# Kernel optimization log

Hardware: AMD Instinct MI355X
Metric: run time of the kernel (lower is better)

The kernel has to match this reference:

```python
import jax, jax.numpy as jnp
import numpy as np

# Material / problem parameters (from init_kwargs)
G_C = 0.0027
L_0 = 0.015
PF_TOL = 0.01
ENERGY_SCALING = 1.0
NU = 0.3
E_MOD = 210.0
LAM = E_MOD * NU / ((1.0 + NU) * (1.0 - 2.0 * NU))
MU = E_MOD / (2.0 * (1.0 + NU))
K_MOD = LAM + 2.0 * MU / 3.0  # bulk modulus for vol/dev split

N_NODES = 263169
N_ELEMS = 262144
N_IP = 4
NN = 4  # nodes per element


def setup_inputs() -> dict:
    key = jax.random.key(0)
    ks = jax.random.split(key, 9)
    u = jax.random.normal(ks[0], (N_NODES,), dtype=jnp.float32) * 0.01
    v = jax.random.normal(ks[1], (N_NODES,), dtype=jnp.float32) * 0.01
    c = jax.random.uniform(ks[2], (N_NODES,), dtype=jnp.float32)
    prev_c = jax.random.uniform(ks[3], (N_NODES,), dtype=jnp.float32)
    connectivities = jax.random.randint(ks[4], (N_ELEMS, NN), 0, N_NODES, dtype=jnp.int32)
    N = jax.random.uniform(ks[5], (N_ELEMS, N_IP, NN), dtype=jnp.float32)
    N = N / jnp.sum(N, axis=-1, keepdims=True)  # shape functions sum to 1
    dNdx = jax.random.normal(ks[6], (N_ELEMS, N_IP, 2, NN), dtype=jnp.float32)
    B = jax.random.normal(ks[7], (N_ELEMS, N_IP, 3, 2 * NN), dtype=jnp.float32)
    volumes = jax.random.uniform(ks[8], (N_ELEMS, N_IP), dtype=jnp.float32)
    return {"u": u, "v": v, "c": c, "prev_c": prev_c,
            "connectivities": connectivities, "N": N, "dNdx": dNdx,
            "B": B, "volumes": volumes}


def reference(u, v, c, prev_c, connectivities, N, dNdx, B, volumes):
    # --- phase-field gather + degradation -------------------------------
    c_el = c[connectivities]                     # [E, nn] irregular gather
    one_minus_c_el = 1.0 - c_el                  # c_elemental in source
    one_minus_c_ip = jnp.einsum('ein,en->ei', N, one_minus_c_el)  # [E, ip]
    ip_g = one_minus_c_ip ** 2                   # degradation g = (1-c)^2

    # --- fracture (AT2) energy density ----------------------------------
    c_ip = 1.0 - one_minus_c_ip
    grad_c = jnp.einsum('eidn,en->eid', dNdx, c_el)  # [E, ip, 2]
    frac_density = (G_C / (2.0 * L_0)) * (c_ip ** 2 + (L_0 ** 2) * jnp.sum(grad_c ** 2, axis=-1))
    E_fracture = jnp.sum(frac_density * volumes)

    # --- irreversibility penalty ----------------------------------------
    penalty = G_C / L_0 * (1.0 / PF_TOL ** 2 - 1.0) * ENERGY_SCALING
    E_irr = jnp.sum(0.5 * penalty * jax.nn.relu(prev_c - c) ** 2)

    # --- B-matrix strain transform --------------------------------------
    u_el = u[connectivities]                     # [E, nn]
    v_el = v[connectivities]                     # [E, nn]
    uv = jnp.stack((u_el, v_el), axis=-1).reshape(u_el.shape[0], 2 * NN)  # interleaved dofs
    strain = jnp.einsum('eikn,en->eik', B, uv)   # Voigt [E, ip, 3]
    exx, eyy, gxy = strain[..., 0], strain[..., 1], strain[..., 2]
    exy = 0.5 * gxy
    tr = exx + eyy                               # plane strain: ezz = 0

    # --- vol/dev (Amor) split energy parts ------------------------------
    dev_xx = exx - tr / 3.0
    dev_yy = eyy - tr / 3.0
    dev_zz = -tr / 3.0
    dev2 = dev_xx ** 2 + dev_yy ** 2 + dev_zz ** 2 + 2.0 * exy ** 2
    tr_pos = jnp.maximum(tr, 0.0)
    tr_neg = jnp.minimum(tr, 0.0)
    psi_plus = 0.5 * K_MOD * tr_pos ** 2 + MU * dev2
    psi_minus = 0.5 * K_MOD * tr_neg ** 2

    ip_strain_energy = (psi_plus * ip_g + psi_minus) * volumes
    E_elastic = jnp.sum(ip_strain_energy)
    return (E_elastic, E_fracture, E_irr)
```

## Files before the change

kernel.cpp:

```cpp
#include <hip/hip_runtime.h>

namespace {
constexpr int N_ELEMS  = 262144;
constexpr int N_NODES  = 263169;
constexpr int BLK      = 256;
constexpr int EPB      = 64;
constexpr int NBLOCKS  = N_ELEMS / EPB;
constexpr int PACK_BLOCKS = (N_NODES + BLK - 1) / BLK;

constexpr long long WS2_F4   = 263232;
constexpr long long P_EL_OFF = WS2_F4 * 4;
constexpr long long P_IR_OFF = P_EL_OFF + 2LL * NBLOCKS;

constexpr float GC_2L0  = 0.09f;
constexpr float L0SQ    = 0.015f * 0.015f;
constexpr float MU_     = 80.76923076923077f;
constexpr float K_MOD   = 175.0f;
constexpr float PENALTY = 1799.82f;
}

typedef float vfloat4 __attribute__((ext_vector_type(4)));

__device__ __forceinline__ float waveReduce(float x) {
#pragma unroll
    for (int off = 32; off; off >>= 1) x += __shfl_down(x, off, 64);
    return x;
}

__global__ __launch_bounds__(256) void pack_nodes(
    const float* __restrict__ u, const float* __restrict__ v,
    const float* __restrict__ c, const float* __restrict__ prev_c,
    float* __restrict__ ws2, float* __restrict__ partialsI)
{
    const int i = blockIdx.x * BLK + threadIdx.x;
    float Eirr = 0.f;
    if (i < N_NODES) {
        const float ci = c[i], ui = u[i], vi = v[i];
        const float d = fmaxf(prev_c[i] - ci, 0.f);
        Eirr = 0.5f * PENALTY * d * d;
        vfloat4 r; r.x = ci; r.y = ui; r.z = vi; r.w = 0.f;
        __builtin_nontemporal_store(r, reinterpret_cast<vfloat4*>(ws2) + i);
    }
    Eirr = waveReduce(Eirr);
    __shared__ float sI[4];
    const int lane = threadIdx.x & 63, wid = threadIdx.x >> 6;
    if (lane == 0) sI[wid] = Eirr;
    __syncthreads();
    if (threadIdx.x == 0)
        partialsI[blockIdx.x] = sI[0] + sI[1] + sI[2] + sI[3];
}

__global__ __launch_bounds__(256) void fused_energy(
    const int* __restrict__ conn,
    const float* __restrict__ Nf, const float* __restrict__ dNdx,
    const float* __restrict__ B, const float* __restrict__ vol,
    const float* __restrict__ ws2, float* __restrict__ partials)
{
    __shared__ vfloat4 ldsB[24 * 65];
    __shared__ vfloat4 ldsD[2 * 257];

    const int k     = threadIdx.x;
    const int ebase = blockIdx.x * EPB;
    const vfloat4* Bf4 = reinterpret_cast<const vfloat4*>(B);
    const vfloat4* Df4 = reinterpret_cast<const vfloat4*>(dNdx);
    const vfloat4* Nf4 = reinterpret_cast<const vfloat4*>(Nf);
    const vfloat4* W4  = reinterpret_cast<const vfloat4*>(ws2);

    const vfloat4* Bg = Bf4 + (long long)ebase * 24;
#pragma unroll
    for (int r = 0; r < 6; ++r) {
        const int j = k + BLK * r;
        ldsB[(j % 24) * 65 + (j / 24)] = Bg[j];
    }
    const vfloat4* Dg = Df4 + (long long)ebase * 8;
#pragma unroll
    for (int r = 0; r < 2; ++r) {
        const int j = k + BLK * r;
        ldsD[(j & 1) * 257 + (j >> 1)] = Dg[j];
    }

    const int idx = conn[4ll * ebase + k];
    const vfloat4 nv = W4[idx];

    const vfloat4 Nr  = Nf4[4ll * ebase + k];
    const float   vip = vol[4ll * ebase + k];

    const int base = k & ~3;
    const float c0 = __shfl(nv.x, base),     c1 = __shfl(nv.x, base + 1);
    const float c2 = __shfl(nv.x, base + 2), c3 = __shfl(nv.x, base + 3);
    const float u0 = __shfl(nv.y, base),     u1 = __shfl(nv.y, base + 1);
    const float u2 = __shfl(nv.y, base + 2), u3 = __shfl(nv.y, base + 3);
    const float v0 = __shfl(nv.z, base),     v1 = __shfl(nv.z, base + 1);
    const float v2 = __shfl(nv.z, base + 2), v3 = __shfl(nv.z, base + 3);

    __syncthreads();

    const int m = k >> 2, ip = k & 3;
    const vfloat4 dx = ldsD[k], dy = ldsD[257 + k];
    const vfloat4 b0 = ldsB[(6 * ip + 0) * 65 + m];
    const vfloat4 b1 = ldsB[(6 * ip + 1) * 65 + m];
    const vfloat4 b2 = ldsB[(6 * ip + 2) * 65 + m];
    const vfloat4 b3 = ldsB[(6 * ip + 3) * 65 + m];
    const vfloat4 b4 = ldsB[(6 * ip + 4) * 65 + m];
    const vfloat4 b5 = ldsB[(6 * ip + 5) * 65 + m];

    const float o0 = 1.f - c0, o1 = 1.f - c1, o2 = 1.f - c2, o3 = 1.f - c3;
    const float omc = Nr.x * o0 + Nr.y * o1 + Nr.z * o2 + Nr.w * o3;
    const float g   = omc * omc;
    const float cip = 1.f - omc;
    const float gx  = dx.x * c0 + dx.y * c1 + dx.z * c2 + dx.w * c3;
    const float gy  = dy.x * c0 + dy.y * c1 + dy.z * c2 + dy.w * c3;
    float Efr = GC_2L0 * (cip * cip + L0SQ * (gx * gx + gy * gy)) * vip;

    const float exx = b0.x * u0 + b0.y * v0 + b0.z * u1 + b0.w * v1
                    + b1.x * u2 + b1.y * v2 + b1.z * u3 + b1.w * v3;
    const float eyy = b2.x * u0 + b2.y * v0 + b2.z * u1 + b2.w * v1
                    + b3.x * u2 + b3.y * v2 + b3.z * u3 + b3.w * v3;
    const float gxy = b4.x * u0 + b4.y * v0 + b4.z * u1 + b4.w * v1
                    + b5.x * u2 + b5.y * v2 + b5.z * u3 + b5.w * v3;
    const float exy = 0.5f * gxy;
    const float tr  = exx + eyy, tr3 = tr * (1.f / 3.f);
    const float dxx = exx - tr3, dyy = eyy - tr3, dzz = -tr3;
    const float dev2 = dxx * dxx + dyy * dyy + dzz * dzz + 2.f * exy * exy;
    const float trp = fmaxf(tr, 0.f), trn = fminf(tr, 0.f);
    float Eel = ((0.5f * K_MOD * trp * trp + MU_ * dev2) * g
                 + 0.5f * K_MOD * trn * trn) * vip;

    Eel = waveReduce(Eel);
    Efr = waveReduce(Efr);
    __shared__ float sE[4], sF[4];
    const int lane = k & 63, wid = k >> 6;
    if (lane == 0) { sE[wid] = Eel; sF[wid] = Efr; }
    __syncthreads();
    if (k == 0) {
        float* p = partials + 2ll * blockIdx.x;
        p[0] = sE[0] + sE[1] + sE[2] + sE[3];
        p[1] = sF[0] + sF[1] + sF[2] + sF[3];
    }
}

__global__ __launch_bounds__(256) void final_reduce(
    const float* __restrict__ partials, const float* __restrict__ partialsI,
    float* __restrict__ out)
{
    float s0 = 0.f, s1 = 0.f, s2 = 0.f;
    for (int i = threadIdx.x; i < NBLOCKS; i += 256) {
        s0 += partials[2ll * i];
        s1 += partials[2ll * i + 1];
    }
    for (int i = threadIdx.x; i < PACK_BLOCKS; i += 256)
        s2 += partialsI[i];
    s0 = waveReduce(s0);
    s1 = waveReduce(s1);
    s2 = waveReduce(s2);
    __shared__ float sA[4], sB[4], sC[4];
    const int lane = threadIdx.x & 63, wid = threadIdx.x >> 6;
    if (lane == 0) { sA[wid] = s0; sB[wid] = s1; sC[wid] = s2; }
    __syncthreads();
    if (threadIdx.x == 0) {
        out[0] = sA[0] + sA[1] + sA[2] + sA[3];
        out[1] = sB[0] + sB[1] + sB[2] + sB[3];
        out[2] = sC[0] + sC[1] + sC[2] + sC[3];
    }
}

extern "C" void kernel_launch(void* const* d_in, const int* in_sizes, int n_in,
                              void* d_out, int out_size, void* d_ws, size_t ws_size,
                              hipStream_t stream) {
    const float* u      = (const float*)d_in[0];
    const float* v      = (const float*)d_in[1];
    const float* c      = (const float*)d_in[2];
    const float* prev_c = (const float*)d_in[3];
    const int*   conn   = (const int*)d_in[4];
    const float* Nf     = (const float*)d_in[5];
    const float* dNdx   = (const float*)d_in[6];
    const float* B      = (const float*)d_in[7];
    const float* vol    = (const float*)d_in[8];
    float* out = (float*)d_out;

    float* ws2       = (float*)d_ws;
    float* partials  = ws2 + P_EL_OFF;
    float* partialsI = ws2 + P_IR_OFF;

    pack_nodes<<<PACK_BLOCKS, BLK, 0, stream>>>(u, v, c, prev_c, ws2, partialsI);
    fused_energy<<<NBLOCKS, BLK, 0, stream>>>(conn, Nf, dNdx, B, vol, ws2, partials);
    final_reduce<<<1, BLK, 0, stream>>>(partials, partialsI, out);
}
```

Baseline: 50.48 us.

## Move connectivity gather into pre-pass writing per-element SoA node values

The first kernel now performs the irregular connectivity gather itself, reading c, u and v at each connected node and writing them per element into a 12-float workspace record. The energy kernel becomes a purely streaming grid-stride loop with direct per-thread vector loads of B and dNdx, replacing the LDS transposition and wave shuffles. Both kernels use a fixed 1024-block grid. The cost is an extra 12 MB workspace write plus read-back, and three scattered scalar gathers instead of one 16-byte gather. Per-thread B loads are strided by 96 bytes, so they coalesce less well than before.

Result: slower. 52.85 us (+4.7%).

```diff
diff --git a/kernel.cpp b/kernel.cpp
--- a/kernel.cpp
+++ b/kernel.cpp
@@ -1,16 +1,16 @@
 #include <hip/hip_runtime.h>
 
 namespace {
-constexpr int N_ELEMS  = 262144;
-constexpr int N_NODES  = 263169;
-constexpr int BLK      = 256;
-constexpr int EPB      = 64;
-constexpr int NBLOCKS  = N_ELEMS / EPB;
-constexpr int PACK_BLOCKS = (N_NODES + BLK - 1) / BLK;
+constexpr int N_ELEMS = 262144;
+constexpr int N_NODES = 263169;
+constexpr int N_UNITS = N_ELEMS * 4;
+constexpr int BLK     = 256;
+constexpr int GRID1   = 1024;
+constexpr int GRID2   = 1024;
 
-constexpr long long WS2_F4   = 263232;
-constexpr long long P_EL_OFF = WS2_F4 * 4;
-constexpr long long P_IR_OFF = P_EL_OFF + 2LL * NBLOCKS;
+constexpr long long WSP_F    = 12LL * N_ELEMS;
+constexpr long long P2_OFF   = WSP_F;
+constexpr long long PI_OFF   = P2_OFF + 2LL * GRID2;
 
 constexpr float GC_2L0  = 0.09f;
 constexpr float L0SQ    = 0.015f * 0.015f;
@@ -27,20 +27,30 @@
     return x;
 }
 
-__global__ __launch_bounds__(256) void pack_nodes(
+__global__ __launch_bounds__(256) void gather_pack(
     const float* __restrict__ u, const float* __restrict__ v,
     const float* __restrict__ c, const float* __restrict__ prev_c,
-    float* __restrict__ ws2, float* __restrict__ partialsI)
+    const int* __restrict__ conn,
+    float* __restrict__ wsP, float* __restrict__ partialsI)
 {
-    const int i = blockIdx.x * BLK + threadIdx.x;
+    const int t0 = blockIdx.x * BLK + threadIdx.x;
+    const int stride = GRID1 * BLK;
+
     float Eirr = 0.f;
-    if (i < N_NODES) {
-        const float ci = c[i], ui = u[i], vi = v[i];
-        const float d = fmaxf(prev_c[i] - ci, 0.f);
-        Eirr = 0.5f * PENALTY * d * d;
-        vfloat4 r; r.x = ci; r.y = ui; r.z = vi; r.w = 0.f;
-        __builtin_nontemporal_store(r, reinterpret_cast<vfloat4*>(ws2) + i);
+    for (int n = t0; n < N_NODES; n += stride) {
+        const float d = fmaxf(prev_c[n] - c[n], 0.f);
+        Eirr += 0.5f * PENALTY * d * d;
     }
+
+    for (int w = t0; w < N_UNITS; w += stride) {
+        const int e  = w >> 2;
+        const int ip = w & 3;
+        const int idx = conn[w];
+        wsP[12 * e + ip]     = c[idx];
+        wsP[12 * e + 4 + ip] = u[idx];
+        wsP[12 * e + 8 + ip] = v[idx];
+    }
+
     Eirr = waveReduce(Eirr);
     __shared__ float sI[4];
     const int lane = threadIdx.x & 63, wid = threadIdx.x >> 6;
@@ -50,89 +60,65 @@
         partialsI[blockIdx.x] = sI[0] + sI[1] + sI[2] + sI[3];
 }
 
-__global__ __launch_bounds__(256) void fused_energy(
-    const int* __restrict__ conn,
+__global__ __launch_bounds__(256) void stream_energy(
+    const float* __restrict__ wsP,
     const float* __restrict__ Nf, const float* __restrict__ dNdx,
     const float* __restrict__ B, const float* __restrict__ vol,
-    const float* __restrict__ ws2, float* __restrict__ partials)
+    float* __restrict__ partials)
 {
-    __shared__ vfloat4 ldsB[24 * 65];
-    __shared__ vfloat4 ldsD[2 * 257];
+    const vfloat4* W   = reinterpret_cast<const vfloat4*>(wsP);
+    const vfloat4* Nf4 = reinterpret_cast<const vfloat4*>(Nf);
+    const vfloat4* Df4 = reinterpret_cast<const vfloat4*>(dNdx);
+    const vfloat4* Bf4 = reinterpret_cast<const vfloat4*>(B);
 
-    const int k     = threadIdx.x;
-    const int ebase = blockIdx.x * EPB;
-    const vfloat4* Bf4 = reinterpret_cast<const vfloat4*>(B);
-    const vfloat4* Df4 = reinterpret_cast<const vfloat4*>(dNdx);
-    const vfloat4* Nf4 = reinterpret_cast<const vfloat4*>(Nf);
-    const vfloat4* W4  = reinterpret_cast<const vfloat4*>(ws2);
+    float Eel = 0.f, Efr = 0.f;
 
-    const vfloat4* Bg = Bf4 + (long long)ebase * 24;
-#pragma unroll
-    for (int r = 0; r < 6; ++r) {
-        const int j = k + BLK * r;
-        ldsB[(j % 24) * 65 + (j / 24)] = Bg[j];
+    for (int unit = blockIdx.x * BLK + threadIdx.x; unit < N_UNITS;
+         unit += GRID2 * BLK) {
+        const int e = unit >> 2;
+
+        const vfloat4 cv = W[3 * e];
+        const vfloat4 uv = W[3 * e + 1];
+        const vfloat4 vv = W[3 * e + 2];
+        const vfloat4 Nr = Nf4[unit];
+        const vfloat4 dx = Df4[2 * unit];
+        const vfloat4 dy = Df4[2 * unit + 1];
+        const long long b6 = 6LL * unit;
+        const vfloat4 b0 = Bf4[b6 + 0], b1 = Bf4[b6 + 1], b2 = Bf4[b6 + 2];
+        const vfloat4 b3 = Bf4[b6 + 3], b4 = Bf4[b6 + 4], b5 = Bf4[b6 + 5];
+        const float  vip = vol[unit];
+
+        const float o0 = 1.f - cv.x, o1 = 1.f - cv.y;
+        const float o2 = 1.f - cv.z, o3 = 1.f - cv.w;
+        const float omc = Nr.x * o0 + Nr.y * o1 + Nr.z * o2 + Nr.w * o3;
+        const float g   = omc * omc;
+        const float cip = 1.f - omc;
+        const float gx  = dx.x * cv.x + dx.y * cv.y + dx.z * cv.z + dx.w * cv.w;
+        const float gy  = dy.x * cv.x + dy.y * cv.y + dy.z * cv.z + dy.w * cv.w;
+        Efr += GC_2L0 * (cip * cip + L0SQ * (gx * gx + gy * gy)) * vip;
+
+        const float exx = b0.x * uv.x + b0.y * vv.x + b0.z * uv.y + b0.w * vv.y
+                        + b1.x * uv.z + b1.y * vv.z + b1.z * uv.w + b1.w * vv.w;
+        const float eyy = b2.x * uv.x + b2.y * vv.x + b2.z * uv.y + b2.w * vv.y
+                        + b3.x * uv.z + b3.y * vv.z + b3.z * uv.w + b3.w * vv.w;
+        const float gxy = b4.x * uv.x + b4.y * vv.x + b4.z * uv.y + b4.w * vv.y
+                        + b5.x * uv.z + b5.y * vv.z + b5.z * uv.w + b5.w * vv.w;
+        const float exy = 0.5f * gxy;
+        const float tr  = exx + eyy, tr3 = tr * (1.f / 3.f);
+        const float dxx = exx - tr3, dyy = eyy - tr3, dzz = -tr3;
+        const float dev2 = dxx * dxx + dyy * dyy + dzz * dzz + 2.f * exy * exy;
+        const float trp = fmaxf(tr, 0.f), trn = fminf(tr, 0.f);
+        Eel += ((0.5f * K_MOD * trp * trp + MU_ * dev2) * g
+                + 0.5f * K_MOD * trn * trn) * vip;
     }
-    const vfloat4* Dg = Df4 + (long long)ebase * 8;
-#pragma unroll
-    for (int r = 0; r < 2; ++r) {
-        const int j = k + BLK * r;
-        ldsD[(j & 1) * 257 + (j >> 1)] = Dg[j];
-    }
-
-    const int idx = conn[4ll * ebase + k];
-    const vfloat4 nv = W4[idx];
-
-    const vfloat4 Nr  = Nf4[4ll * ebase + k];
-    const float   vip = vol[4ll * ebase + k];
-
-    const int base = k & ~3;
-    const float c0 = __shfl(nv.x, base),     c1 = __shfl(nv.x, base + 1);
-    const float c2 = __shfl(nv.x, base + 2), c3 = __shfl(nv.x, base + 3);
-    const float u0 = __shfl(nv.y, base),     u1 = __shfl(nv.y, base + 1);
-    const float u2 = __shfl(nv.y, base + 2), u3 = __shfl(nv.y, base + 3);
-    const float v0 = __shfl(nv.z, base),     v1 = __shfl(nv.z, base + 1);
-    const float v2 = __shfl(nv.z, base + 2), v3 = __shfl(nv.z, base + 3);
-
-    __syncthreads();
-
-    const int m = k >> 2, ip = k & 3;
-    const vfloat4 dx = ldsD[k], dy = ldsD[257 + k];
-    const vfloat4 b0 = ldsB[(6 * ip + 0) * 65 + m];
-    const vfloat4 b1 = ldsB[(6 * ip + 1) * 65 + m];
-    const vfloat4 b2 = ldsB[(6 * ip + 2) * 65 + m];
-    const vfloat4 b3 = ldsB[(6 * ip + 3) * 65 + m];
-    const vfloat4 b4 = ldsB[(6 * ip + 4) * 65 + m];
-    const vfloat4 b5 = ldsB[(6 * ip + 5) * 65 + m];
-
-    const float o0 = 1.f - c0, o1 = 1.f - c1, o2 = 1.f - c2, o3 = 1.f - c3;
-    const float omc = Nr.x * o0 + Nr.y * o1 + Nr.z * o2 + Nr.w * o3;
-    const float g   = omc * omc;
-    const float cip = 1.f - omc;
-    const float gx  = dx.x * c0 + dx.y * c1 + dx.z * c2 + dx.w * c3;
-    const float gy  = dy.x * c0 + dy.y * c1 + dy.z * c2 + dy.w * c3;
-    float Efr = GC_2L0 * (cip * cip + L0SQ * (gx * gx + gy * gy)) * vip;
-
-    const float exx = b0.x * u0 + b0.y * v0 + b0.z * u1 + b0.w * v1
-                    + b1.x * u2 + b1.y * v2 + b1.z * u3 + b1.w * v3;
-    const float eyy = b2.x * u0 + b2.y * v0 + b2.z * u1 + b2.w * v1
-                    + b3.x * u2 + b3.y * v2 + b3.z * u3 + b3.w * v3;
-    const float gxy = b4.x * u0 + b4.y * v0 + b4.z * u1 + b4.w * v1
-                    + b5.x * u2 + b5.y * v2 + b5.z * u3 + b5.w * v3;
-    const float exy = 0.5f * gxy;
-    const float tr  = exx + eyy, tr3 = tr * (1.f / 3.f);
-    const float dxx = exx - tr3, dyy = eyy - tr3, dzz = -tr3;
-    const float dev2 = dxx * dxx + dyy * dyy + dzz * dzz + 2.f * exy * exy;
-    const float trp = fmaxf(tr, 0.f), trn = fminf(tr, 0.f);
-    float Eel = ((0.5f * K_MOD * trp * trp + MU_ * dev2) * g
-                 + 0.5f * K_MOD * trn * trn) * vip;
 
     Eel = waveReduce(Eel);
     Efr = waveReduce(Efr);
     __shared__ float sE[4], sF[4];
-    const int lane = k & 63, wid = k >> 6;
+    const int lane = threadIdx.x & 63, wid = threadIdx.x >> 6;
     if (lane == 0) { sE[wid] = Eel; sF[wid] = Efr; }
     __syncthreads();
-    if (k == 0) {
+    if (threadIdx.x == 0) {
         float* p = partials + 2ll * blockIdx.x;
         p[0] = sE[0] + sE[1] + sE[2] + sE[3];
         p[1] = sF[0] + sF[1] + sF[2] + sF[3];
@@ -144,11 +130,11 @@
     float* __restrict__ out)
 {
     float s0 = 0.f, s1 = 0.f, s2 = 0.f;
-    for (int i = threadIdx.x; i < NBLOCKS; i += 256) {
+    for (int i = threadIdx.x; i < GRID2; i += 256) {
         s0 += partials[2ll * i];
         s1 += partials[2ll * i + 1];
     }
-    for (int i = threadIdx.x; i < PACK_BLOCKS; i += 256)
+    for (int i = threadIdx.x; i < GRID1; i += 256)
         s2 += partialsI[i];
     s0 = waveReduce(s0);
     s1 = waveReduce(s1);
@@ -178,11 +164,11 @@
     const float* vol    = (const float*)d_in[8];
     float* out = (float*)d_out;
 
-    float* ws2       = (float*)d_ws;
-    float* partials  = ws2 + P_EL_OFF;
-    float* partialsI = ws2 + P_IR_OFF;
+    float* wsP       = (float*)d_ws;
+    float* partials  = wsP + P2_OFF;
+    float* partialsI = wsP + PI_OFF;
 
-    pack_nodes<<<PACK_BLOCKS, BLK, 0, stream>>>(u, v, c, prev_c, ws2, partialsI);
-    fused_energy<<<NBLOCKS, BLK, 0, stream>>>(conn, Nf, dNdx, B, vol, ws2, partials);
+    gather_pack<<<GRID1, BLK, 0, stream>>>(u, v, c, prev_c, conn, wsP, partialsI);
+    stream_energy<<<GRID2, BLK, 0, stream>>>(wsP, Nf, dNdx, B, vol, partials);
     final_reduce<<<1, BLK, 0, stream>>>(partials, partialsI, out);
 }
```
